# Kernel tuning notes

Measured on AMD Instinct MI355X. Metric: run time of the kernel, lower is better.

The kernel has to match this reference:

```python
import jax, jax.numpy as jnp
import numpy as np

HID = 64
PRE = 14


def _lstm_last(x, Wih, Whh, b):
    # x: (B, T, F) batch_first; single-layer torch LSTM; returns last hidden (B, H)
    H = Whh.shape[1]
    def step(carry, xt):
        h, c = carry
        g = xt @ Wih.T + h @ Whh.T + b  # gates order i,f,g,o (torch convention)
        i, f, gg, o = jnp.split(g, 4, axis=-1)
        c = jax.nn.sigmoid(f) * c + jax.nn.sigmoid(i) * jnp.tanh(gg)
        h = jax.nn.sigmoid(o) * jnp.tanh(c)
        return (h, c), None
    h0 = jnp.zeros((x.shape[0], H), x.dtype)
    (h, _), _ = jax.lax.scan(step, (h0, h0), jnp.swapaxes(x, 0, 1))
    return h


def _sircell(beta, gamma, c, sir):
    # beta,gamma: (B,N,1); c: (B,N,N); sir: (B,N,3); beta_incorporated=False branch
    eps = 1e-8
    S, I, R = sir[..., 0:1], sir[..., 1:2], sir[..., 2:3]
    Ntot = jnp.maximum(S + I + R, eps)
    infection = c @ I                      # (B,N,1) graph diffusion of infected
    dS = -beta * S / Ntot * infection
    dI = -dS - gamma * I
    dR = gamma * I
    S_t = jnp.maximum(S + dS, 0.0)
    I_t = jnp.maximum(I + dI, 0.0)
    R_t = jnp.maximum(R + dR, 0.0)
    scale = Ntot / jnp.maximum(S_t + I_t + R_t, eps)
    I_new = jnp.maximum(-dS, 0.0)
    return jnp.concatenate([I_new, S_t * scale, I_t * scale, R_t * scale], axis=-1)


def reference(x_s, x, bWih, bWhh, bb, bfW, bfb, gWih, gWhh, gb, gfW, gfb, cWih, cWhh, cb, cfW, cfb):
    B, T, N, F = x_s.shape
    P = bfW.shape[0]
    xs = jnp.transpose(x_s, (0, 2, 1, 3)).reshape(B * N, T, F)
    betas = jax.nn.sigmoid(_lstm_last(xs, bWih, bWhh, bb) @ bfW.T + bfb).reshape(B, N, P, 1)
    gammas = jax.nn.sigmoid(_lstm_last(xs, gWih, gWhh, gb) @ gfW.T + gfb).reshape(B, N, P, 1)
    xst = jnp.transpose(x_s, (0, 2, 1, 3))                       # (B,N,T,F)
    Hi = jnp.broadcast_to(xst[:, :, None], (B, N, N, T, F))
    Hj = jnp.broadcast_to(xst[:, None], (B, N, N, T, F))
    edge = jnp.concatenate([Hi, Hj], -1).reshape(B * N * N, T, 2 * F)
    cij = jax.nn.sigmoid(_lstm_last(edge, cWih, cWhh, cb) @ cfW.T + cfb).reshape(B, N, N, P)
    cij = jax.nn.softmax(jnp.transpose(cij, (0, 3, 1, 2)), axis=-1)  # (B,P,N,N)
    cs = jnp.transpose(cij, (0, 2, 1, 3))                            # (B,N,P,N)

    def step(sir, inp):
        bt, gt, ct = inp
        nsir = _sircell(bt, gt, ct, sir)
        return nsir[:, :, 1:], nsir

    _, outs = jax.lax.scan(
        step, x[:, -1],
        (jnp.transpose(betas, (2, 0, 1, 3)),
         jnp.transpose(gammas, (2, 0, 1, 3)),
         jnp.transpose(cs, (2, 0, 1, 3))))
    out = jnp.transpose(outs, (1, 0, 2, 3))                          # (B,P,N,4)
    epi = jnp.transpose(jnp.concatenate([betas, gammas, cs], -1), (0, 2, 1, 3))  # (B,P,N,N+2)
    return out[..., 2:3], epi, out[..., 1:], out[..., 0:1]


def setup_inputs() -> dict:
    key = jax.random.key(0)
    ks = jax.random.split(key, 20)
    B, T, N, F = 4, 12, 128, 3
    H, P = HID, PRE
    s = 1.0 / np.sqrt(H)
    def u(k, shape):
        return jax.random.uniform(k, shape, jnp.float32, -s, s)
    inp = {
        'x_s': jax.random.normal(ks[0], (B, T, N, F), jnp.float32),
        'x': jax.random.uniform(ks[1], (B, T, N, F), jnp.float32),
        'bWih': u(ks[2], (4 * H, F)), 'bWhh': u(ks[3], (4 * H, H)), 'bb': u(ks[4], (4 * H,)),
        'bfW': u(ks[5], (P, H)), 'bfb': u(ks[6], (P,)),
        'gWih': u(ks[7], (4 * H, F)), 'gWhh': u(ks[8], (4 * H, H)), 'gb': u(ks[9], (4 * H,)),
        'gfW': u(ks[10], (P, H)), 'gfb': u(ks[11], (P,)),
        'cWih': u(ks[12], (4 * H, 2 * F)), 'cWhh': u(ks[13], (4 * H, H)), 'cb': u(ks[14], (4 * H,)),
        'cfW': u(ks[15], (P, H)), 'cfb': u(ks[16], (P,)),
    }
    return inp
```

## Files before the change

### kernel.cpp

```cpp
#include <hip/hip_runtime.h>

#define TT 12
#define NN 128
#define BB 4
#define PP 14

typedef __attribute__((ext_vector_type(8))) short short8;
typedef __attribute__((ext_vector_type(4))) float f32x4;
typedef __attribute__((ext_vector_type(2))) float float2v;
typedef __attribute__((ext_vector_type(2))) unsigned uint2v;

__device__ inline unsigned short f2bf(float x){
  unsigned u = __builtin_bit_cast(unsigned, x);
  u += 0x7fffu + ((u >> 16) & 1u);
  return (unsigned short)(u >> 16);
}
__device__ inline float bf2f(unsigned short h){
  unsigned u = ((unsigned)h) << 16;
  return __builtin_bit_cast(float, u);
}
__device__ inline float fexp2(float x){ return __builtin_amdgcn_exp2f(x); }
__device__ inline float sigf(float x){ return __builtin_amdgcn_rcpf(1.0f + fexp2(x * -1.44269504f)); }

__device__ inline float2v exp2v(float2v x){
  float2v r; r[0]=__builtin_amdgcn_exp2f(x[0]); r[1]=__builtin_amdgcn_exp2f(x[1]); return r;
}
__device__ inline float2v rcpv(float2v x){
  float2v r; r[0]=__builtin_amdgcn_rcpf(x[0]); r[1]=__builtin_amdgcn_rcpf(x[1]); return r;
}
__device__ inline float2v sig2(float2v x){ return rcpv(1.0f + exp2v(x * -1.44269504f)); }
__device__ inline float2v tanh2(float2v x){ return 1.0f - 2.0f*rcpv(1.0f + exp2v(x * 2.88539008f)); }

__global__ __launch_bounds__(256) void lstm_all(
    const float* __restrict__ x_s,
    const float* __restrict__ bWih, const float* __restrict__ bWhh, const float* __restrict__ bb_,
    const float* __restrict__ bfW,  const float* __restrict__ bfb,
    const float* __restrict__ gWih, const float* __restrict__ gWhh, const float* __restrict__ gb_,
    const float* __restrict__ gfW,  const float* __restrict__ gfb,
    const float* __restrict__ cWih, const float* __restrict__ cWhh, const float* __restrict__ cb_,
    const float* __restrict__ cfW,  const float* __restrict__ cfb,
    float* __restrict__ out_epi,
    float* __restrict__ betas_ws, float* __restrict__ gammas_ws)
{
  __shared__ __align__(16) char hbuf[2*2048];
  __shared__ __align__(16) unsigned short xext[TT*16*8];
  __shared__ float fw_lds[PP*64];
  __shared__ float fb_lds[PP];

  const int tid = threadIdx.x;
  const int l = tid & 63, w = tid >> 6;
  const int col = l & 15, q = l >> 4;

  int g = blockIdx.x;
  int mode; const float *Wih, *Whh, *bias, *fW, *fb;
  if (g < 4096)      { mode=0; Wih=cWih; Whh=cWhh; bias=cb_; fW=cfW; fb=cfb; }
  else if (g < 4128) { mode=1; g-=4096; Wih=bWih; Whh=bWhh; bias=bb_; fW=bfW; fb=bfb; }
  else               { mode=2; g-=4128; Wih=gWih; Whh=gWhh; bias=gb_; fW=gfW; fb=gfb; }

  int b, i=0, j0=0, n0=0;
  if (mode==0) { b = g >> 10; int rem = g & 1023; i = rem >> 3; j0 = (rem & 7) << 4; }
  else         { b = g >> 3; n0 = (g & 7) << 4; }

  for (int task = tid; task < TT*16; task += 256) {
    int t = task >> 4, m = task & 15;
    unsigned short* dst = &xext[(t*16+m)*8];
    float v0=0,v1=0,v2=0,v3=0,v4=0,v5=0,v6=0,v7=0;
    if (mode==0) {
      const float* xi = x_s + ((b*TT + t)*NN + i)*3;
      const float* xj = x_s + ((b*TT + t)*NN + (j0+m))*3;
      v0=xi[0]; v1=xi[1]; v2=xi[2]; v3=xj[0]; v4=xj[1]; v5=xj[2]; v6=1.f;
    } else {
      const float* xn = x_s + ((b*TT + t)*NN + (n0+m))*3;
      v0=xn[0]; v1=xn[1]; v2=xn[2]; v3=1.f;
    }
    dst[0]=f2bf(v0); dst[1]=f2bf(v1); dst[2]=f2bf(v2); dst[3]=f2bf(v3);
    dst[4]=f2bf(v4); dst[5]=f2bf(v5); dst[6]=f2bf(v6); dst[7]=f2bf(v7);
  }
  for (int idx = tid; idx < 512; idx += 256) ((unsigned*)hbuf)[idx] = 0;
  for (int idx = tid; idx < PP*64; idx += 256) fw_lds[idx] = fW[idx];
  if (tid < PP) fb_lds[tid] = fb[tid];

  short8 Aw[4][2]; short8 Ax[4];
  #pragma unroll
  for (int gt = 0; gt < 4; ++gt) {
    int gate = gt*64 + w*16 + col;
    #pragma unroll
    for (int kt = 0; kt < 2; ++kt) {
      const float* src = Whh + gate*64 + kt*32 + q*8;
      short8 fr;
      #pragma unroll
      for (int jj = 0; jj < 8; ++jj) fr[jj] = (short)f2bf(src[jj]);
      Aw[gt][kt] = fr;
    }
    short8 ax = {0,0,0,0,0,0,0,0};
    if (q == 0) {
      if (mode==0) {
        ax[0]=(short)f2bf(Wih[gate*6+0]); ax[1]=(short)f2bf(Wih[gate*6+1]); ax[2]=(short)f2bf(Wih[gate*6+2]);
        ax[3]=(short)f2bf(Wih[gate*6+3]); ax[4]=(short)f2bf(Wih[gate*6+4]); ax[5]=(short)f2bf(Wih[gate*6+5]);
        ax[6]=(short)f2bf(bias[gate]);
      } else {
        ax[0]=(short)f2bf(Wih[gate*3+0]); ax[1]=(short)f2bf(Wih[gate*3+1]); ax[2]=(short)f2bf(Wih[gate*3+2]);
        ax[3]=(short)f2bf(bias[gate]);
      }
    }
    Ax[gt] = ax;
  }

  __syncthreads();

  const int rot = (col & 7) << 4;
  const int r0off = col*128 + ((  0 + (q<<4) + rot) & 127);
  const int r1off = col*128 + (( 64 + (q<<4) + rot) & 127);
  const int wroff = col*128 + ((w*32 + q*8 + rot) & 127);

  float2v c0 = {0.f,0.f}, c1 = {0.f,0.f};
  const short8 zero8 = {0,0,0,0,0,0,0,0};

  for (int t = 0; t < TT; ++t) {
    const char* rb = hbuf + ((t & 1) ? 2048 : 0);
    char* wbp      = hbuf + ((t & 1) ? 0 : 2048);
    short8 b0 = *(const short8*)(rb + r0off);
    short8 b1 = *(const short8*)(rb + r1off);
    short8 bx = zero8;
    if (l < 16) bx = *(const short8*)&xext[(t*16 + col)*8];
    f32x4 A0 = {0.f,0.f,0.f,0.f}, A1 = A0, A2 = A0, A3 = A0;
    A0 = __builtin_amdgcn_mfma_f32_16x16x32_bf16(Aw[0][0], b0, A0, 0,0,0);
    A0 = __builtin_amdgcn_mfma_f32_16x16x32_bf16(Aw[0][1], b1, A0, 0,0,0);
    A0 = __builtin_amdgcn_mfma_f32_16x16x32_bf16(Ax[0],    bx, A0, 0,0,0);
    A1 = __builtin_amdgcn_mfma_f32_16x16x32_bf16(Aw[1][0], b0, A1, 0,0,0);
    A1 = __builtin_amdgcn_mfma_f32_16x16x32_bf16(Aw[1][1], b1, A1, 0,0,0);
    A1 = __builtin_amdgcn_mfma_f32_16x16x32_bf16(Ax[1],    bx, A1, 0,0,0);
    A2 = __builtin_amdgcn_mfma_f32_16x16x32_bf16(Aw[2][0], b0, A2, 0,0,0);
    A2 = __builtin_amdgcn_mfma_f32_16x16x32_bf16(Aw[2][1], b1, A2, 0,0,0);
    A2 = __builtin_amdgcn_mfma_f32_16x16x32_bf16(Ax[2],    bx, A2, 0,0,0);
    A3 = __builtin_amdgcn_mfma_f32_16x16x32_bf16(Aw[3][0], b0, A3, 0,0,0);
    A3 = __builtin_amdgcn_mfma_f32_16x16x32_bf16(Aw[3][1], b1, A3, 0,0,0);
    A3 = __builtin_amdgcn_mfma_f32_16x16x32_bf16(Ax[3],    bx, A3, 0,0,0);

    float2v i0 = {A0[0],A0[1]}, i1 = {A0[2],A0[3]};
    float2v f0 = {A1[0],A1[1]}, f1 = {A1[2],A1[3]};
    float2v g0 = {A2[0],A2[1]}, g1 = {A2[2],A2[3]};
    float2v o0 = {A3[0],A3[1]}, o1 = {A3[2],A3[3]};
    c0 = sig2(f0)*c0 + sig2(i0)*tanh2(g0);
    c1 = sig2(f1)*c1 + sig2(i1)*tanh2(g1);
    float2v h0 = sig2(o0)*tanh2(c0);
    float2v h1 = sig2(o1)*tanh2(c1);
    unsigned plo, phi;
    asm("v_cvt_pk_bf16_f32 %0, %1, %2" : "=v"(plo) : "v"(h0[0]), "v"(h0[1]));
    asm("v_cvt_pk_bf16_f32 %0, %1, %2" : "=v"(phi) : "v"(h1[0]), "v"(h1[1]));
    uint2v pv = {plo, phi};
    *(uint2v*)(wbp + wroff) = pv;
    __syncthreads();
  }

  const char* hfin = hbuf;
  for (int task = tid; task < 16*PP; task += 256) {
    int seq = task & 15, p = task >> 4;
    int rot2 = (seq & 7) << 4;
    float dot = fb_lds[p];
    #pragma unroll
    for (int kc = 0; kc < 8; ++kc) {
      short8 v = *(const short8*)(hfin + seq*128 + (((kc<<4) + rot2) & 127));
      #pragma unroll
      for (int jj = 0; jj < 8; ++jj)
        dot += bf2f((unsigned short)v[jj]) * fw_lds[p*64 + kc*8 + jj];
    }
    float val = sigf(dot);
    if (mode==0) {
      out_epi[(size_t)((b*PP + p)*NN + i)*130 + 2 + (j0+seq)] = val;
    } else if (mode==1) {
      betas_ws[(b*NN + n0+seq)*PP + p] = val;
    } else {
      gammas_ws[(b*NN + n0+seq)*PP + p] = val;
    }
  }
}

__global__ __launch_bounds__(256) void softmax_epi(
    const float* __restrict__ betas_ws, const float* __restrict__ gammas_ws,
    float* __restrict__ out_epi)
{
  int row = blockIdx.x*4 + (threadIdx.x >> 6);
  int l = threadIdx.x & 63;
  int b = row / (PP*NN); int rem = row - b*(PP*NN); int p = rem >> 7; int i = rem & 127;
  float* epi = out_epi + (size_t)row*130;
  float v0 = epi[2+l], v1 = epi[2+64+l];
  float m = fmaxf(v0, v1);
  #pragma unroll
  for (int off = 32; off; off >>= 1) m = fmaxf(m, __shfl_xor(m, off));
  float e0 = fexp2((v0-m)*1.44269504f), e1 = fexp2((v1-m)*1.44269504f);
  float s = e0 + e1;
  #pragma unroll
  for (int off = 32; off; off >>= 1) s += __shfl_xor(s, off);
  float inv = 1.0f / s;
  epi[2+l] = e0*inv; epi[2+64+l] = e1*inv;
  if (l == 0) epi[0] = betas_ws[(b*NN+i)*PP + p];
  if (l == 1) epi[1] = gammas_ws[(b*NN+i)*PP + p];
}

__global__ __launch_bounds__(1024) void sir_scan(
    const float* __restrict__ x,
    const float* __restrict__ betas_ws, const float* __restrict__ gammas_ws,
    const float* __restrict__ epi,
    float* __restrict__ out0, float* __restrict__ out2, float* __restrict__ out3)
{
  __shared__ float Ish[NN];
  int b = blockIdx.x;
  int tid = threadIdx.x;
  int i = tid >> 3, q = tid & 7;
  const float* x0 = x + ((b*TT + 11)*NN + i)*3;
  float S = x0[0], I = x0[1], R = x0[2];
  if (q == 0) Ish[i] = I;
  __syncthreads();
  for (int p = 0; p < PP; ++p) {
    const float* crow = epi + (size_t)((b*PP + p)*NN + i)*130 + 2 + q*16;
    float part = 0.f;
    #pragma unroll
    for (int jj = 0; jj < 8; ++jj) {
      float2v v = *(const float2v*)(crow + jj*2);
      part += v[0]*Ish[q*16 + jj*2] + v[1]*Ish[q*16 + jj*2 + 1];
    }
    part += __shfl_xor(part, 1);
    part += __shfl_xor(part, 2);
    part += __shfl_xor(part, 4);
    __syncthreads();
    if (q == 0) {
      float beta  = betas_ws[(b*NN+i)*PP + p];
      float gamma = gammas_ws[(b*NN+i)*PP + p];
      float Ntot = fmaxf(S+I+R, 1e-8f);
      float dS = -beta*S/Ntot*part;
      float dI = -dS - gamma*I;
      float dR = gamma*I;
      float St = fmaxf(S+dS, 0.f), It = fmaxf(I+dI, 0.f), Rt = fmaxf(R+dR, 0.f);
      float scale = Ntot / fmaxf(St+It+Rt, 1e-8f);
      float Inew = fmaxf(-dS, 0.f);
      int o = (b*PP+p)*NN + i;
      float Sn = St*scale, In = It*scale, Rn = Rt*scale;
      out0[o] = In;
      out2[o*3+0] = Sn; out2[o*3+1] = In; out2[o*3+2] = Rn;
      out3[o] = Inew;
      S = Sn; I = In; R = Rn;
      Ish[i] = I;
    }
    __syncthreads();
  }
}

extern "C" void kernel_launch(void* const* d_in, const int* in_sizes, int n_in,
                              void* d_out, int out_size, void* d_ws, size_t ws_size,
                              hipStream_t stream) {
  const float* x_s  = (const float*)d_in[0];
  const float* x    = (const float*)d_in[1];
  const float* bWih = (const float*)d_in[2];
  const float* bWhh = (const float*)d_in[3];
  const float* bb_  = (const float*)d_in[4];
  const float* bfW  = (const float*)d_in[5];
  const float* bfb  = (const float*)d_in[6];
  const float* gWih = (const float*)d_in[7];
  const float* gWhh = (const float*)d_in[8];
  const float* gb_  = (const float*)d_in[9];
  const float* gfW  = (const float*)d_in[10];
  const float* gfb  = (const float*)d_in[11];
  const float* cWih = (const float*)d_in[12];
  const float* cWhh = (const float*)d_in[13];
  const float* cb_  = (const float*)d_in[14];
  const float* cfW  = (const float*)d_in[15];
  const float* cfb  = (const float*)d_in[16];

  float* out  = (float*)d_out;
  float* out0 = out;
  float* epi  = out + 7168;
  float* out2 = out + 7168 + 931840;
  float* out3 = out + 7168 + 931840 + 21504;
  float* betas_ws  = (float*)d_ws;
  float* gammas_ws = betas_ws + 7168;

  hipLaunchKernelGGL(lstm_all, dim3(4160), dim3(256), 0, stream,
      x_s, bWih,bWhh,bb_,bfW,bfb, gWih,gWhh,gb_,gfW,gfb, cWih,cWhh,cb_,cfW,cfb,
      epi, betas_ws, gammas_ws);
  hipLaunchKernelGGL(softmax_epi, dim3(1792), dim3(256), 0, stream,
      betas_ws, gammas_ws, epi);
  hipLaunchKernelGGL(sir_scan, dim3(4), dim3(1024), 0, stream,
      x, betas_ws, gammas_ws, epi, out0, out2, out3);
}
```

Measured before the change: 114.6 us.

## Fold activation scales into weights, process two tiles per block, prefetch SIR rows

```diff
diff --git a/kernel.cpp b/kernel.cpp
--- a/kernel.cpp
+++ b/kernel.cpp
@@ -28,8 +28,8 @@
 __device__ inline float2v rcpv(float2v x){
   float2v r; r[0]=__builtin_amdgcn_rcpf(x[0]); r[1]=__builtin_amdgcn_rcpf(x[1]); return r;
 }
-__device__ inline float2v sig2(float2v x){ return rcpv(1.0f + exp2v(x * -1.44269504f)); }
-__device__ inline float2v tanh2(float2v x){ return 1.0f - 2.0f*rcpv(1.0f + exp2v(x * 2.88539008f)); }
+__device__ inline float2v sigp(float2v xp){ return rcpv(1.0f + exp2v(xp)); }
+__device__ inline float2v tanhp(float2v xp){ return 1.0f - 2.0f*rcpv(1.0f + exp2v(xp)); }
 
 __global__ __launch_bounds__(256) void lstm_all(
     const float* __restrict__ x_s,
@@ -51,127 +51,140 @@
   const int l = tid & 63, w = tid >> 6;
   const int col = l & 15, q = l >> 4;
 
-  int g = blockIdx.x;
-  int mode; const float *Wih, *Whh, *bias, *fW, *fb;
-  if (g < 4096)      { mode=0; Wih=cWih; Whh=cWhh; bias=cb_; fW=cfW; fb=cfb; }
-  else if (g < 4128) { mode=1; g-=4096; Wih=bWih; Whh=bWhh; bias=bb_; fW=bfW; fb=bfb; }
-  else               { mode=2; g-=4128; Wih=gWih; Whh=gWhh; bias=gb_; fW=gfW; fb=gfb; }
-
-  int b, i=0, j0=0, n0=0;
-  if (mode==0) { b = g >> 10; int rem = g & 1023; i = rem >> 3; j0 = (rem & 7) << 4; }
-  else         { b = g >> 3; n0 = (g & 7) << 4; }
-
-  for (int task = tid; task < TT*16; task += 256) {
-    int t = task >> 4, m = task & 15;
-    unsigned short* dst = &xext[(t*16+m)*8];
-    float v0=0,v1=0,v2=0,v3=0,v4=0,v5=0,v6=0,v7=0;
-    if (mode==0) {
-      const float* xi = x_s + ((b*TT + t)*NN + i)*3;
-      const float* xj = x_s + ((b*TT + t)*NN + (j0+m))*3;
-      v0=xi[0]; v1=xi[1]; v2=xi[2]; v3=xj[0]; v4=xj[1]; v5=xj[2]; v6=1.f;
-    } else {
-      const float* xn = x_s + ((b*TT + t)*NN + (n0+m))*3;
-      v0=xn[0]; v1=xn[1]; v2=xn[2]; v3=1.f;
-    }
-    dst[0]=f2bf(v0); dst[1]=f2bf(v1); dst[2]=f2bf(v2); dst[3]=f2bf(v3);
-    dst[4]=f2bf(v4); dst[5]=f2bf(v5); dst[6]=f2bf(v6); dst[7]=f2bf(v7);
-  }
-  for (int idx = tid; idx < 512; idx += 256) ((unsigned*)hbuf)[idx] = 0;
-  for (int idx = tid; idx < PP*64; idx += 256) fw_lds[idx] = fW[idx];
-  if (tid < PP) fb_lds[tid] = fb[tid];
-
-  short8 Aw[4][2]; short8 Ax[4];
-  #pragma unroll
-  for (int gt = 0; gt < 4; ++gt) {
-    int gate = gt*64 + w*16 + col;
-    #pragma unroll
-    for (int kt = 0; kt < 2; ++kt) {
-      const float* src = Whh + gate*64 + kt*32 + q*8;
-      short8 fr;
-      #pragma unroll
-      for (int jj = 0; jj < 8; ++jj) fr[jj] = (short)f2bf(src[jj]);
-      Aw[gt][kt] = fr;
-    }
-    short8 ax = {0,0,0,0,0,0,0,0};
-    if (q == 0) {
-      if (mode==0) {
-        ax[0]=(short)f2bf(Wih[gate*6+0]); ax[1]=(short)f2bf(Wih[gate*6+1]); ax[2]=(short)f2bf(Wih[gate*6+2]);
-        ax[3]=(short)f2bf(Wih[gate*6+3]); ax[4]=(short)f2bf(Wih[gate*6+4]); ax[5]=(short)f2bf(Wih[gate*6+5]);
-        ax[6]=(short)f2bf(bias[gate]);
-      } else {
-        ax[0]=(short)f2bf(Wih[gate*3+0]); ax[1]=(short)f2bf(Wih[gate*3+1]); ax[2]=(short)f2bf(Wih[gate*3+2]);
-        ax[3]=(short)f2bf(bias[gate]);
-      }
-    }
-    Ax[gt] = ax;
-  }
-
-  __syncthreads();
-
   const int rot = (col & 7) << 4;
   const int r0off = col*128 + ((  0 + (q<<4) + rot) & 127);
   const int r1off = col*128 + (( 64 + (q<<4) + rot) & 127);
   const int wroff = col*128 + ((w*32 + q*8 + rot) & 127);
 
-  float2v c0 = {0.f,0.f}, c1 = {0.f,0.f};
+  short8 Aw[4][2]; short8 Ax[4];
+  int pmode = -1;
   const short8 zero8 = {0,0,0,0,0,0,0,0};
 
-  for (int t = 0; t < TT; ++t) {
-    const char* rb = hbuf + ((t & 1) ? 2048 : 0);
-    char* wbp      = hbuf + ((t & 1) ? 0 : 2048);
-    short8 b0 = *(const short8*)(rb + r0off);
-    short8 b1 = *(const short8*)(rb + r1off);
-    short8 bx = zero8;
-    if (l < 16) bx = *(const short8*)&xext[(t*16 + col)*8];
-    f32x4 A0 = {0.f,0.f,0.f,0.f}, A1 = A0, A2 = A0, A3 = A0;
-    A0 = __builtin_amdgcn_mfma_f32_16x16x32_bf16(Aw[0][0], b0, A0, 0,0,0);
-    A0 = __builtin_amdgcn_mfma_f32_16x16x32_bf16(Aw[0][1], b1, A0, 0,0,0);
-    A0 = __builtin_amdgcn_mfma_f32_16x16x32_bf16(Ax[0],    bx, A0, 0,0,0);
-    A1 = __builtin_amdgcn_mfma_f32_16x16x32_bf16(Aw[1][0], b0, A1, 0,0,0);
-    A1 = __builtin_amdgcn_mfma_f32_16x16x32_bf16(Aw[1][1], b1, A1, 0,0,0);
-    A1 = __builtin_amdgcn_mfma_f32_16x16x32_bf16(Ax[1],    bx, A1, 0,0,0);
-    A2 = __builtin_amdgcn_mfma_f32_16x16x32_bf16(Aw[2][0], b0, A2, 0,0,0);
-    A2 = __builtin_amdgcn_mfma_f32_16x16x32_bf16(Aw[2][1], b1, A2, 0,0,0);
-    A2 = __builtin_amdgcn_mfma_f32_16x16x32_bf16(Ax[2],    bx, A2, 0,0,0);
-    A3 = __builtin_amdgcn_mfma_f32_16x16x32_bf16(Aw[3][0], b0, A3, 0,0,0);
-    A3 = __builtin_amdgcn_mfma_f32_16x16x32_bf16(Aw[3][1], b1, A3, 0,0,0);
-    A3 = __builtin_amdgcn_mfma_f32_16x16x32_bf16(Ax[3],    bx, A3, 0,0,0);
-
-    float2v i0 = {A0[0],A0[1]}, i1 = {A0[2],A0[3]};
-    float2v f0 = {A1[0],A1[1]}, f1 = {A1[2],A1[3]};
-    float2v g0 = {A2[0],A2[1]}, g1 = {A2[2],A2[3]};
-    float2v o0 = {A3[0],A3[1]}, o1 = {A3[2],A3[3]};
-    c0 = sig2(f0)*c0 + sig2(i0)*tanh2(g0);
-    c1 = sig2(f1)*c1 + sig2(i1)*tanh2(g1);
-    float2v h0 = sig2(o0)*tanh2(c0);
-    float2v h1 = sig2(o1)*tanh2(c1);
-    unsigned plo, phi;
-    asm("v_cvt_pk_bf16_f32 %0, %1, %2" : "=v"(plo) : "v"(h0[0]), "v"(h0[1]));
-    asm("v_cvt_pk_bf16_f32 %0, %1, %2" : "=v"(phi) : "v"(h1[0]), "v"(h1[1]));
-    uint2v pv = {plo, phi};
-    *(uint2v*)(wbp + wroff) = pv;
+  for (int it = 0; it < 2; ++it) {
+    int g = blockIdx.x + it*2080;
+
+    int mode; const float *Wih, *Whh, *bias, *fW, *fb;
+    if (g < 4096)      { mode=0; Wih=cWih; Whh=cWhh; bias=cb_; fW=cfW; fb=cfb; }
+    else if (g < 4128) { mode=1; g-=4096; Wih=bWih; Whh=bWhh; bias=bb_; fW=bfW; fb=bfb; }
+    else               { mode=2; g-=4128; Wih=gWih; Whh=gWhh; bias=gb_; fW=gfW; fb=gfb; }
+
+    int b, i=0, j0=0, n0=0;
+    if (mode==0) { b = g >> 10; int rem = g & 1023; i = rem >> 3; j0 = (rem & 7) << 4; }
+    else         { b = g >> 3; n0 = (g & 7) << 4; }
+
     __syncthreads();
-  }
-
-  const char* hfin = hbuf;
-  for (int task = tid; task < 16*PP; task += 256) {
-    int seq = task & 15, p = task >> 4;
-    int rot2 = (seq & 7) << 4;
-    float dot = fb_lds[p];
-    #pragma unroll
-    for (int kc = 0; kc < 8; ++kc) {
-      short8 v = *(const short8*)(hfin + seq*128 + (((kc<<4) + rot2) & 127));
+
+    if (mode != pmode) {
+      pmode = mode;
+      for (int idx = tid; idx < PP*64; idx += 256) fw_lds[idx] = fW[idx];
+      if (tid < PP) fb_lds[tid] = fb[tid];
       #pragma unroll
-      for (int jj = 0; jj < 8; ++jj)
-        dot += bf2f((unsigned short)v[jj]) * fw_lds[p*64 + kc*8 + jj];
-    }
-    float val = sigf(dot);
-    if (mode==0) {
-      out_epi[(size_t)((b*PP + p)*NN + i)*130 + 2 + (j0+seq)] = val;
-    } else if (mode==1) {
-      betas_ws[(b*NN + n0+seq)*PP + p] = val;
-    } else {
-      gammas_ws[(b*NN + n0+seq)*PP + p] = val;
+      for (int gt = 0; gt < 4; ++gt) {
+        float sc = (gt==2) ? 2.88539008f : -1.44269504f;
+        int gate = gt*64 + w*16 + col;
+        #pragma unroll
+        for (int kt = 0; kt < 2; ++kt) {
+          const float* src = Whh + gate*64 + kt*32 + q*8;
+          short8 fr;
+          #pragma unroll
+          for (int jj = 0; jj < 8; ++jj) fr[jj] = (short)f2bf(src[jj]*sc);
+          Aw[gt][kt] = fr;
+        }
+        short8 ax = {0,0,0,0,0,0,0,0};
+        if (q == 0) {
+          if (mode==0) {
+            ax[0]=(short)f2bf(Wih[gate*6+0]*sc); ax[1]=(short)f2bf(Wih[gate*6+1]*sc); ax[2]=(short)f2bf(Wih[gate*6+2]*sc);
+            ax[3]=(short)f2bf(Wih[gate*6+3]*sc); ax[4]=(short)f2bf(Wih[gate*6+4]*sc); ax[5]=(short)f2bf(Wih[gate*6+5]*sc);
+            ax[6]=(short)f2bf(bias[gate]*sc);
+          } else {
+            ax[0]=(short)f2bf(Wih[gate*3+0]*sc); ax[1]=(short)f2bf(Wih[gate*3+1]*sc); ax[2]=(short)f2bf(Wih[gate*3+2]*sc);
+            ax[3]=(short)f2bf(bias[gate]*sc);
+          }
+        }
+        Ax[gt] = ax;
+      }
+    }
+
+    for (int task = tid; task < TT*16; task += 256) {
+      int t = task >> 4, m = task & 15;
+      unsigned short* dst = &xext[(t*16+m)*8];
+      float v0=0,v1=0,v2=0,v3=0,v4=0,v5=0,v6=0,v7=0;
+      if (mode==0) {
+        const float* xi = x_s + ((b*TT + t)*NN + i)*3;
+        const float* xj = x_s + ((b*TT + t)*NN + (j0+m))*3;
+        v0=xi[0]; v1=xi[1]; v2=xi[2]; v3=xj[0]; v4=xj[1]; v5=xj[2]; v6=1.f;
+      } else {
+        const float* xn = x_s + ((b*TT + t)*NN + (n0+m))*3;
+        v0=xn[0]; v1=xn[1]; v2=xn[2]; v3=1.f;
+      }
+      dst[0]=f2bf(v0); dst[1]=f2bf(v1); dst[2]=f2bf(v2); dst[3]=f2bf(v3);
+      dst[4]=f2bf(v4); dst[5]=f2bf(v5); dst[6]=f2bf(v6); dst[7]=f2bf(v7);
+    }
+    for (int idx = tid; idx < 512; idx += 256) ((unsigned*)hbuf)[idx] = 0;
+
+    __syncthreads();
+
+    float2v c0 = {0.f,0.f}, c1 = {0.f,0.f};
+
+    for (int t = 0; t < TT; ++t) {
+      const char* rb = hbuf + ((t & 1) ? 2048 : 0);
+      char* wbp      = hbuf + ((t & 1) ? 0 : 2048);
+      short8 b0 = *(const short8*)(rb + r0off);
+      short8 b1 = *(const short8*)(rb + r1off);
+      short8 bx = zero8;
+      if (l < 16) bx = *(const short8*)&xext[(t*16 + col)*8];
+      f32x4 Fi = {0.f,0.f,0.f,0.f}, Ii = Fi, Gi = Fi, Oi = Fi;
+      Fi = __builtin_amdgcn_mfma_f32_16x16x32_bf16(Aw[1][0], b0, Fi, 0,0,0);
+      Fi = __builtin_amdgcn_mfma_f32_16x16x32_bf16(Aw[1][1], b1, Fi, 0,0,0);
+      Fi = __builtin_amdgcn_mfma_f32_16x16x32_bf16(Ax[1],    bx, Fi, 0,0,0);
+      Ii = __builtin_amdgcn_mfma_f32_16x16x32_bf16(Aw[0][0], b0, Ii, 0,0,0);
+      Ii = __builtin_amdgcn_mfma_f32_16x16x32_bf16(Aw[0][1], b1, Ii, 0,0,0);
+      Ii = __builtin_amdgcn_mfma_f32_16x16x32_bf16(Ax[0],    bx, Ii, 0,0,0);
+      Gi = __builtin_amdgcn_mfma_f32_16x16x32_bf16(Aw[2][0], b0, Gi, 0,0,0);
+      Gi = __builtin_amdgcn_mfma_f32_16x16x32_bf16(Aw[2][1], b1, Gi, 0,0,0);
+      Gi = __builtin_amdgcn_mfma_f32_16x16x32_bf16(Ax[2],    bx, Gi, 0,0,0);
+      Oi = __builtin_amdgcn_mfma_f32_16x16x32_bf16(Aw[3][0], b0, Oi, 0,0,0);
+      Oi = __builtin_amdgcn_mfma_f32_16x16x32_bf16(Aw[3][1], b1, Oi, 0,0,0);
+      Oi = __builtin_amdgcn_mfma_f32_16x16x32_bf16(Ax[3],    bx, Oi, 0,0,0);
+
+      float2v f0 = {Fi[0],Fi[1]}, f1 = {Fi[2],Fi[3]};
+      float2v i0 = {Ii[0],Ii[1]}, i1 = {Ii[2],Ii[3]};
+      float2v g0 = {Gi[0],Gi[1]}, g1 = {Gi[2],Gi[3]};
+      float2v o0 = {Oi[0],Oi[1]}, o1 = {Oi[2],Oi[3]};
+      c0 = sigp(f0)*c0 + sigp(i0)*tanhp(g0);
+      c1 = sigp(f1)*c1 + sigp(i1)*tanhp(g1);
+      float2v tc0 = 1.0f - 2.0f*rcpv(1.0f + exp2v(c0 * 2.88539008f));
+      float2v tc1 = 1.0f - 2.0f*rcpv(1.0f + exp2v(c1 * 2.88539008f));
+      float2v h0 = sigp(o0)*tc0;
+      float2v h1 = sigp(o1)*tc1;
+      unsigned plo, phi;
+      asm("v_cvt_pk_bf16_f32 %0, %1, %2" : "=v"(plo) : "v"(h0[0]), "v"(h0[1]));
+      asm("v_cvt_pk_bf16_f32 %0, %1, %2" : "=v"(phi) : "v"(h1[0]), "v"(h1[1]));
+      uint2v pv = {plo, phi};
+      *(uint2v*)(wbp + wroff) = pv;
+      __syncthreads();
+    }
+
+    const char* hfin = hbuf;
+    for (int task = tid; task < 16*PP; task += 256) {
+      int seq = task & 15, p = task >> 4;
+      int rot2 = (seq & 7) << 4;
+      float dot = fb_lds[p];
+      #pragma unroll
+      for (int kc = 0; kc < 8; ++kc) {
+        short8 v = *(const short8*)(hfin + seq*128 + (((kc<<4) + rot2) & 127));
+        #pragma unroll
+        for (int jj = 0; jj < 8; ++jj)
+          dot += bf2f((unsigned short)v[jj]) * fw_lds[p*64 + kc*8 + jj];
+      }
+      float val = sigf(dot);
+      if (mode==0) {
+        out_epi[(size_t)((b*PP + p)*NN + i)*130 + 2 + (j0+seq)] = val;
+      } else if (mode==1) {
+        betas_ws[(b*NN + n0+seq)*PP + p] = val;
+      } else {
+        gammas_ws[(b*NN + n0+seq)*PP + p] = val;
+      }
     }
   }
 }
@@ -211,15 +224,24 @@
   const float* x0 = x + ((b*TT + 11)*NN + i)*3;
   float S = x0[0], I = x0[1], R = x0[2];
   if (q == 0) Ish[i] = I;
+
+  float2v v[8], vn[8];
+  {
+    const float* crow = epi + (size_t)((b*PP + 0)*NN + i)*130 + 2 + q*16;
+    #pragma unroll
+    for (int jj = 0; jj < 8; ++jj) v[jj] = *(const float2v*)(crow + jj*2);
+  }
   __syncthreads();
   for (int p = 0; p < PP; ++p) {
-    const float* crow = epi + (size_t)((b*PP + p)*NN + i)*130 + 2 + q*16;
+    if (p+1 < PP) {
+      const float* crow = epi + (size_t)((b*PP + p+1)*NN + i)*130 + 2 + q*16;
+      #pragma unroll
+      for (int jj = 0; jj < 8; ++jj) vn[jj] = *(const float2v*)(crow + jj*2);
+    }
     float part = 0.f;
     #pragma unroll
-    for (int jj = 0; jj < 8; ++jj) {
-      float2v v = *(const float2v*)(crow + jj*2);
-      part += v[0]*Ish[q*16 + jj*2] + v[1]*Ish[q*16 + jj*2 + 1];
-    }
+    for (int jj = 0; jj < 8; ++jj)
+      part += v[jj][0]*Ish[q*16 + jj*2] + v[jj][1]*Ish[q*16 + jj*2 + 1];
     part += __shfl_xor(part, 1);
     part += __shfl_xor(part, 2);
     part += __shfl_xor(part, 4);
@@ -242,6 +264,8 @@
       S = Sn; I = In; R = Rn;
       Ish[i] = I;
     }
+    #pragma unroll
+    for (int jj = 0; jj < 8; ++jj) v[jj] = vn[jj];
     __syncthreads();
   }
 }
@@ -275,7 +299,7 @@
   float* betas_ws  = (float*)d_ws;
   float* gammas_ws = betas_ws + 7168;
 
-  hipLaunchKernelGGL(lstm_all, dim3(4160), dim3(256), 0, stream,
+  hipLaunchKernelGGL(lstm_all, dim3(2080), dim3(256), 0, stream,
       x_s, bWih,bWhh,bb_,bfW,bfb, gWih,gWhh,gb_,gfW,gfb, cWih,cWhh,cb_,cfW,cfb,
       epi, betas_ws, gammas_ws);
   hipLaunchKernelGGL(softmax_epi, dim3(1792), dim3(256), 0, stream,
```

Measured after the change: 120.0 us. 4.7% more time.
